# Optimization experiments

Measured on AMD Instinct MI355X. Metric: run time of the kernel, lower is better.

Reference implementation:

```python
import jax, jax.numpy as jnp
import numpy as np

B, S, D = 2, 2048, 768
H = 12
HD = D // H  # 64
SCALE = HD ** -0.5


def setup_inputs() -> dict:
    key = jax.random.key(0)
    k1, k2, k3, k4, k5 = jax.random.split(key, 5)
    x = jax.random.normal(k1, (B, S, D), dtype=jnp.float32)
    w_qkv = jax.random.normal(k2, (D, 3 * D), dtype=jnp.float32) * (D ** -0.5)
    b_qkv = jax.random.normal(k3, (3 * D,), dtype=jnp.float32) * 0.02
    w_proj = jax.random.normal(k4, (D, D), dtype=jnp.float32) * (D ** -0.5)
    b_proj = jax.random.normal(k5, (D,), dtype=jnp.float32) * 0.02
    return {"x": x, "w_qkv": w_qkv, "b_qkv": b_qkv, "w_proj": w_proj, "b_proj": b_proj}


def reference(x, w_qkv, b_qkv, w_proj, b_proj):
    b, s, d = x.shape
    # QKV projection: (B,S,3D) -> (3,B,H,S,HD)
    qkv = x @ w_qkv + b_qkv
    qkv = qkv.reshape(b, s, 3, H, HD).transpose(2, 0, 3, 1, 4)
    q, k, v = qkv[0], qkv[1], qkv[2]
    q = q * SCALE
    # full NxN attention scores, as in the original module
    attn = jnp.einsum("bhqd,bhkd->bhqk", q, k)
    attn = jax.nn.softmax(attn, axis=-1)
    out = jnp.einsum("bhqk,bhkd->bhqd", attn, v)  # (B,H,S,HD)
    out = out.transpose(0, 2, 1, 3).reshape(b, s, d)
    return out @ w_proj + b_proj
```

## Files before the change

### kernel.cpp

```cpp
#include <hip/hip_runtime.h>
#include <hip/hip_bf16.h>

#define B_ 2
#define S_ 2048
#define D_ 768
#define H_ 12
#define HD_ 64
#define EXP2C_ 0.1803368801111244f

typedef __attribute__((ext_vector_type(8))) short bf16x8;
typedef __attribute__((ext_vector_type(8))) unsigned short u16x8;
typedef __attribute__((ext_vector_type(4))) float f32x4;

static __device__ __forceinline__ unsigned short f2bf(float x) {
    union { float f; unsigned u; } v; v.f = x;
    unsigned r = (v.u + 0x7FFFu + ((v.u >> 16) & 1u)) >> 16;
    return (unsigned short)r;
}
static __device__ __forceinline__ float bf2f(unsigned short h) {
    union { unsigned u; float f; } v; v.u = ((unsigned)h) << 16;
    return v.f;
}
static __device__ __forceinline__ float fexp2(float x) { return __builtin_exp2f(x); }

static __device__ __forceinline__ unsigned pk_bf16(float a, float b) {
    __hip_bfloat162 pk = __float22bfloat162_rn(make_float2(a, b));
    union { __hip_bfloat162 h; unsigned u; } v; v.h = pk;
    return v.u;
}

static __device__ __forceinline__ f32x4 mfma32(bf16x8 a, bf16x8 b, f32x4 c) {
    return __builtin_amdgcn_mfma_f32_16x16x32_bf16(a, b, c, 0, 0, 0);
}

typedef __attribute__((address_space(3))) unsigned int lds_u32;
typedef __attribute__((address_space(1))) const unsigned int glb_u32;
static __device__ __forceinline__ void glds16(const unsigned short* g, unsigned short* l) {
    __builtin_amdgcn_global_load_lds((glb_u32*)g, (lds_u32*)l, 16, 0, 0);
}

#define PREP_CONV_ 1536
#define PREP_TQKV_ 1728
#define PREP_TPRJ_ 576
__global__ __launch_bounds__(256) void prep_kernel(
    const float* __restrict__ x,      unsigned short* __restrict__ x16,
    const float* __restrict__ w_qkv,  unsigned short* __restrict__ wqkvT,
    const float* __restrict__ w_proj, unsigned short* __restrict__ wprojT)
{
    __shared__ float tile[32][33];
    const int bid = blockIdx.x, t = threadIdx.x;
    if (bid < PREP_CONV_) {
        const int i = (bid * 256 + t) * 8;
        float4 a0 = *(const float4*)(x + i);
        float4 a1 = *(const float4*)(x + i + 4);
        u16x8 s;
        s[0] = f2bf(a0.x); s[1] = f2bf(a0.y); s[2] = f2bf(a0.z); s[3] = f2bf(a0.w);
        s[4] = f2bf(a1.x); s[5] = f2bf(a1.y); s[6] = f2bf(a1.z); s[7] = f2bf(a1.w);
        *(u16x8*)(x16 + i) = s;
        return;
    }
    const float* w; unsigned short* wT; int N, bb;
    if (bid < PREP_CONV_ + PREP_TQKV_) { w = w_qkv; wT = wqkvT; N = 3 * D_; bb = bid - PREP_CONV_; }
    else                               { w = w_proj; wT = wprojT; N = D_;   bb = bid - PREP_CONV_ - PREP_TQKV_; }
    const int K = D_;
    const int nt = N / 32;
    const int n0 = (bb % nt) * 32, k0 = (bb / nt) * 32;
    const int tx = t & 31, ty = t >> 5;
#pragma unroll
    for (int i = 0; i < 4; i++)
        tile[ty + i * 8][tx] = w[(size_t)(k0 + ty + i * 8) * N + n0 + tx];
    __syncthreads();
#pragma unroll
    for (int i = 0; i < 4; i++)
        wT[(size_t)(n0 + ty + i * 8) * K + k0 + tx] = f2bf(tile[tx][ty + i * 8]);
}

template <int BN, bool OUT_F32>
__global__ __launch_bounds__(256) void gemm_bt_kernel(
    const unsigned short* __restrict__ A,
    const unsigned short* __restrict__ Bt,
    const float* __restrict__ bias,
    void* __restrict__ Cp,
    int M, int N, int K)
{
    __shared__ __align__(16) unsigned short As[128][32];
    __shared__ __align__(16) unsigned short Bs[BN][32];
    constexpr int NJ = BN / 32;

    const int t = threadIdx.x;
    const int w = t >> 6, lane = t & 63, quad = lane >> 4, l16 = lane & 15;
    const int n0 = blockIdx.x * BN, m0 = blockIdx.y * 128;
    const int mw = (w & 1) * 64, nw = (w >> 1) * (BN / 2);

    const f32x4 z = {0.f, 0.f, 0.f, 0.f};
    f32x4 acc[4][NJ];
#pragma unroll
    for (int i = 0; i < 4; i++)
#pragma unroll
        for (int j = 0; j < NJ; j++) acc[i][j] = z;

    for (int kk = 0; kk < K; kk += 32) {
#pragma unroll
        for (int it = 0; it < 2; it++) {
            const int c = t + it * 256, row = c >> 2, c8 = (c & 3) << 3;
            glds16(A + (size_t)(m0 + row) * K + kk + c8, &As[0][0] + c * 8);
        }
#pragma unroll
        for (int it = 0; it < BN / 64; it++) {
            const int c = t + it * 256, row = c >> 2, c8 = (c & 3) << 3;
            glds16(Bt + (size_t)(n0 + row) * K + kk + c8, &Bs[0][0] + c * 8);
        }
        __syncthreads();

        bf16x8 a[4], b[NJ];
#pragma unroll
        for (int i = 0; i < 4; i++)
            a[i] = *(const bf16x8*)(&As[mw + i * 16 + l16][quad * 8]);
#pragma unroll
        for (int j = 0; j < NJ; j++)
            b[j] = *(const bf16x8*)(&Bs[nw + j * 16 + l16][quad * 8]);
#pragma unroll
        for (int i = 0; i < 4; i++)
#pragma unroll
            for (int j = 0; j < NJ; j++)
                acc[i][j] = mfma32(a[i], b[j], acc[i][j]);
        __syncthreads();
    }

#pragma unroll
    for (int j = 0; j < NJ; j++) {
        const int col = n0 + nw + j * 16 + l16;
        const float bv = bias[col];
#pragma unroll
        for (int i = 0; i < 4; i++) {
#pragma unroll
            for (int r = 0; r < 4; r++) {
                const int row = m0 + mw + i * 16 + quad * 4 + r;
                const float v = acc[i][j][r] + bv;
                if (OUT_F32) ((float*)Cp)[(size_t)row * N + col] = v;
                else         ((unsigned short*)Cp)[(size_t)row * N + col] = f2bf(v);
            }
        }
    }
}

__global__ __launch_bounds__(256) void repack_v_kernel(
    const unsigned short* __restrict__ qkv,
    unsigned short* __restrict__ vt)
{
    __shared__ unsigned short T[64][65];
    const int t = threadIdx.x;
    const int bh = blockIdx.x, st = blockIdx.y;
    const int b = bh / H_, h = bh % H_;
    const unsigned short* src =
        qkv + (size_t)(b * S_ + st * 64) * (3 * D_) + 2 * D_ + h * HD_;

#pragma unroll
    for (int it = 0; it < 2; it++) {
        const int c = t + it * 256, sr = c >> 3, g = c & 7;
        u16x8 v = *(const u16x8*)(src + (size_t)sr * (3 * D_) + g * 8);
#pragma unroll
        for (int j = 0; j < 8; j++) T[sr][g * 8 + j] = v[j];
    }
    __syncthreads();
#pragma unroll
    for (int it = 0; it < 2; it++) {
        const int c = t + it * 256, hd = c >> 3, g = c & 7;
        u16x8 v;
#pragma unroll
        for (int j = 0; j < 8; j++) v[j] = T[g * 8 + j][hd];
        *(u16x8*)(vt + (size_t)(bh * HD_ + hd) * S_ + st * 64 + g * 8) = v;
    }
}

__global__ __launch_bounds__(256) void attn_kernel(
    const unsigned short* __restrict__ qkv,
    const unsigned short* __restrict__ vt,
    unsigned short* __restrict__ o)
{
    __shared__ __align__(16) unsigned short Ks[2][64][64];
    __shared__ __align__(16) unsigned short Vs[2][64][64];
    __shared__ __align__(16) unsigned short p_lds[4][16][72];

    const int t = threadIdx.x;
    const int w = t >> 6, lane = t & 63, quad = lane >> 4, l16 = lane & 15;
    const int h8 = l16 & 7;
    const int bh = blockIdx.x, qt = blockIdx.y;
    const int b = bh / H_, h = bh % H_;
    const int ld = 3 * D_;

    const unsigned short* qbase =
        qkv + (size_t)(b * S_ + qt * 64 + 16 * w + l16) * ld + h * HD_;
    u16x8 qr0 = *(const u16x8*)(qbase + quad * 8);
    u16x8 qr1 = *(const u16x8*)(qbase + 32 + quad * 8);
    bf16x8 qf0, qf1;
#pragma unroll
    for (int j = 0; j < 8; j++) {
        qf0[j] = (short)f2bf(bf2f(qr0[j]) * EXP2C_);
        qf1[j] = (short)f2bf(bf2f(qr1[j]) * EXP2C_);
    }

    const unsigned short* kbase = qkv + (size_t)(b * S_) * ld + D_ + h * HD_;
    const unsigned short* vbase = vt + (size_t)bh * HD_ * S_;

    const f32x4 z = {0.f, 0.f, 0.f, 0.f};
    f32x4 o_acc[4] = {z, z, z, z};
    f32x4 l4[4] = {z, z, z, z};

#pragma unroll
    for (int it = 0; it < 2; it++) {
        const int c = t + it * 256, row = c >> 3, g = c & 7, sg = g ^ (row & 7);
        *(u16x8*)(&Ks[0][row][sg * 8]) = *(const u16x8*)(kbase + (size_t)row * ld + g * 8);
        *(u16x8*)(&Vs[0][row][sg * 8]) = *(const u16x8*)(vbase + (size_t)row * S_ + g * 8);
    }
    __syncthreads();

    const int NT = S_ / 64;
    for (int kt = 0; kt < NT; kt++) {
        const int buf = kt & 1;
        const bool pre = (kt + 1 < NT);

        u16x8 pk[2], pv[2];
        if (pre) {
            const int kr1 = (kt + 1) * 64;
#pragma unroll
            for (int i = 0; i < 2; i++) {
                const int c = t + i * 256, row = c >> 3, g = c & 7;
                pk[i] = *(const u16x8*)(kbase + (size_t)(kr1 + row) * ld + g * 8);
                pv[i] = *(const u16x8*)(vbase + (size_t)row * S_ + kr1 + g * 8);
            }
        }

        f32x4 s_acc[4] = {z, z, z, z};
#pragma unroll
        for (int nt = 0; nt < 4; nt++) {
            const unsigned short* kr = &Ks[buf][nt * 16 + l16][0];
            bf16x8 k0 = *(const bf16x8*)(kr + (quad ^ h8) * 8);
            bf16x8 k1 = *(const bf16x8*)(kr + ((quad + 4) ^ h8) * 8);
            s_acc[nt] = mfma32(qf0, k0, s_acc[nt]);
            s_acc[nt] = mfma32(qf1, k1, s_acc[nt]);
        }

#pragma unroll
        for (int nt = 0; nt < 4; nt++) {
            f32x4 pv4;
#pragma unroll
            for (int r = 0; r < 4; r++) pv4[r] = fexp2(s_acc[nt][r]);
            l4[nt] += pv4;
            const unsigned u01 = pk_bf16(pv4[0], pv4[1]);
            const unsigned u23 = pk_bf16(pv4[2], pv4[3]);
            p_lds[w][quad * 4 + 0][nt * 16 + l16] = (unsigned short)u01;
            p_lds[w][quad * 4 + 1][nt * 16 + l16] = (unsigned short)(u01 >> 16);
            p_lds[w][quad * 4 + 2][nt * 16 + l16] = (unsigned short)u23;
            p_lds[w][quad * 4 + 3][nt * 16 + l16] = (unsigned short)(u23 >> 16);
        }
        bf16x8 pa0 = *(const bf16x8*)(&p_lds[w][l16][quad * 8]);
        bf16x8 pa1 = *(const bf16x8*)(&p_lds[w][l16][32 + quad * 8]);

#pragma unroll
        for (int nt = 0; nt < 4; nt++) {
            const int row = nt * 16 + l16;
            bf16x8 v0 = *(const bf16x8*)(&Vs[buf][row][(quad ^ h8) * 8]);
            bf16x8 v1 = *(const bf16x8*)(&Vs[buf][row][((quad + 4) ^ h8) * 8]);
            o_acc[nt] = mfma32(pa0, v0, o_acc[nt]);
            o_acc[nt] = mfma32(pa1, v1, o_acc[nt]);
        }

        if (pre) {
#pragma unroll
            for (int i = 0; i < 2; i++) {
                const int c = t + i * 256, row = c >> 3, g = c & 7, sg = g ^ (row & 7);
                *(u16x8*)(&Ks[buf ^ 1][row][sg * 8]) = pk[i];
                *(u16x8*)(&Vs[buf ^ 1][row][sg * 8]) = pv[i];
            }
        }
        __syncthreads();
    }

#pragma unroll
    for (int r = 0; r < 4; r++) {
        float l = l4[0][r] + l4[1][r] + l4[2][r] + l4[3][r];
        l += __shfl_xor(l, 1, 64); l += __shfl_xor(l, 2, 64);
        l += __shfl_xor(l, 4, 64); l += __shfl_xor(l, 8, 64);
        const float inv = 1.f / l;
        const int row = b * S_ + qt * 64 + 16 * w + quad * 4 + r;
        unsigned short* ob = o + (size_t)row * D_ + h * HD_;
#pragma unroll
        for (int nt = 0; nt < 4; nt++)
            ob[nt * 16 + l16] = f2bf(o_acc[nt][r] * inv);
    }
}

extern "C" void kernel_launch(void* const* d_in, const int* in_sizes, int n_in,
                              void* d_out, int out_size, void* d_ws, size_t ws_size,
                              hipStream_t stream) {
    const float* x      = (const float*)d_in[0];
    const float* w_qkv  = (const float*)d_in[1];
    const float* b_qkv  = (const float*)d_in[2];
    const float* w_proj = (const float*)d_in[3];
    const float* b_proj = (const float*)d_in[4];
    float* out = (float*)d_out;

    unsigned short* qkv    = (unsigned short*)d_ws;
    unsigned short* vtb    = qkv    + (size_t)(B_ * S_) * (3 * D_);
    unsigned short* o_x16  = vtb    + (size_t)(B_ * H_) * HD_ * S_;
    unsigned short* wqkvT  = o_x16  + (size_t)(B_ * S_) * D_;
    unsigned short* wprojT = wqkvT  + (size_t)D_ * (3 * D_);

    dim3 blk(256);
    prep_kernel<<<dim3(PREP_CONV_ + PREP_TQKV_ + PREP_TPRJ_), blk, 0, stream>>>(
        x, o_x16, w_qkv, wqkvT, w_proj, wprojT);
    gemm_bt_kernel<128, false><<<dim3((3 * D_) / 128, (B_ * S_) / 128), blk, 0, stream>>>(
        o_x16, wqkvT, b_qkv, qkv, B_ * S_, 3 * D_, D_);
    repack_v_kernel<<<dim3(B_ * H_, S_ / 64), blk, 0, stream>>>(qkv, vtb);
    attn_kernel<<<dim3(B_ * H_, S_ / 64), blk, 0, stream>>>(qkv, vtb, o_x16);
    gemm_bt_kernel<64, true><<<dim3(D_ / 64, (B_ * S_) / 128), blk, 0, stream>>>(
        o_x16, wprojT, b_proj, out, B_ * S_, D_, D_);
}
```

Baseline: 185.7 us.

## Switch attention to 32x32x16 MFMA with a 2x2 query/key wave split

```diff
diff --git a/kernel.cpp b/kernel.cpp
--- a/kernel.cpp
+++ b/kernel.cpp
@@ -11,26 +11,28 @@
 typedef __attribute__((ext_vector_type(8))) short bf16x8;
 typedef __attribute__((ext_vector_type(8))) unsigned short u16x8;
 typedef __attribute__((ext_vector_type(4))) float f32x4;
+typedef __attribute__((ext_vector_type(16))) float f32x16;
 
 static __device__ __forceinline__ unsigned short f2bf(float x) {
     union { float f; unsigned u; } v; v.f = x;
     unsigned r = (v.u + 0x7FFFu + ((v.u >> 16) & 1u)) >> 16;
     return (unsigned short)r;
 }
+static __device__ __forceinline__ unsigned short f2bf_fast(float x) {
+    union { float f; unsigned u; } v; v.f = x;
+    return (unsigned short)((v.u + 0x8000u) >> 16);
+}
 static __device__ __forceinline__ float bf2f(unsigned short h) {
     union { unsigned u; float f; } v; v.u = ((unsigned)h) << 16;
     return v.f;
 }
 static __device__ __forceinline__ float fexp2(float x) { return __builtin_exp2f(x); }
 
-static __device__ __forceinline__ unsigned pk_bf16(float a, float b) {
-    __hip_bfloat162 pk = __float22bfloat162_rn(make_float2(a, b));
-    union { __hip_bfloat162 h; unsigned u; } v; v.h = pk;
-    return v.u;
-}
-
 static __device__ __forceinline__ f32x4 mfma32(bf16x8 a, bf16x8 b, f32x4 c) {
     return __builtin_amdgcn_mfma_f32_16x16x32_bf16(a, b, c, 0, 0, 0);
+}
+static __device__ __forceinline__ f32x16 mfma3216(bf16x8 a, bf16x8 b, f32x16 c) {
+    return __builtin_amdgcn_mfma_f32_32x32x16_bf16(a, b, c, 0, 0, 0);
 }
 
 typedef __attribute__((address_space(3))) unsigned int lds_u32;
@@ -180,32 +182,31 @@
 {
     __shared__ __align__(16) unsigned short Ks[2][64][64];
     __shared__ __align__(16) unsigned short Vs[2][64][64];
-    __shared__ __align__(16) unsigned short p_lds[4][16][72];
+    __shared__ __align__(16) unsigned short p_lds[4][32][40];
 
     const int t = threadIdx.x;
-    const int w = t >> 6, lane = t & 63, quad = lane >> 4, l16 = lane & 15;
-    const int h8 = l16 & 7;
+    const int w = t >> 6, lane = t & 63;
+    const int l32 = lane & 31, lh = lane >> 5;
+    const int qg = w & 1, kg = w >> 1;
     const int bh = blockIdx.x, qt = blockIdx.y;
     const int b = bh / H_, h = bh % H_;
     const int ld = 3 * D_;
 
-    const unsigned short* qbase =
-        qkv + (size_t)(b * S_ + qt * 64 + 16 * w + l16) * ld + h * HD_;
-    u16x8 qr0 = *(const u16x8*)(qbase + quad * 8);
-    u16x8 qr1 = *(const u16x8*)(qbase + 32 + quad * 8);
-    bf16x8 qf0, qf1;
-#pragma unroll
-    for (int j = 0; j < 8; j++) {
-        qf0[j] = (short)f2bf(bf2f(qr0[j]) * EXP2C_);
-        qf1[j] = (short)f2bf(bf2f(qr1[j]) * EXP2C_);
+    const unsigned short* qb =
+        qkv + (size_t)(b * S_ + qt * 64 + qg * 32 + l32) * ld + h * HD_;
+    bf16x8 qa[4];
+#pragma unroll
+    for (int c = 0; c < 4; c++) {
+        u16x8 r = *(const u16x8*)(qb + c * 16 + lh * 8);
+#pragma unroll
+        for (int j = 0; j < 8; j++) qa[c][j] = (short)f2bf(bf2f(r[j]) * EXP2C_);
     }
 
     const unsigned short* kbase = qkv + (size_t)(b * S_) * ld + D_ + h * HD_;
     const unsigned short* vbase = vt + (size_t)bh * HD_ * S_;
 
-    const f32x4 z = {0.f, 0.f, 0.f, 0.f};
-    f32x4 o_acc[4] = {z, z, z, z};
-    f32x4 l4[4] = {z, z, z, z};
+    f32x16 o0 = {0.f}, o1 = {0.f};
+    f32x4 l4[4] = {{0.f,0.f,0.f,0.f},{0.f,0.f,0.f,0.f},{0.f,0.f,0.f,0.f},{0.f,0.f,0.f,0.f}};
 
 #pragma unroll
     for (int it = 0; it < 2; it++) {
@@ -231,39 +232,41 @@
             }
         }
 
-        f32x4 s_acc[4] = {z, z, z, z};
-#pragma unroll
-        for (int nt = 0; nt < 4; nt++) {
-            const unsigned short* kr = &Ks[buf][nt * 16 + l16][0];
-            bf16x8 k0 = *(const bf16x8*)(kr + (quad ^ h8) * 8);
-            bf16x8 k1 = *(const bf16x8*)(kr + ((quad + 4) ^ h8) * 8);
-            s_acc[nt] = mfma32(qf0, k0, s_acc[nt]);
-            s_acc[nt] = mfma32(qf1, k1, s_acc[nt]);
-        }
-
-#pragma unroll
-        for (int nt = 0; nt < 4; nt++) {
-            f32x4 pv4;
-#pragma unroll
-            for (int r = 0; r < 4; r++) pv4[r] = fexp2(s_acc[nt][r]);
-            l4[nt] += pv4;
-            const unsigned u01 = pk_bf16(pv4[0], pv4[1]);
-            const unsigned u23 = pk_bf16(pv4[2], pv4[3]);
-            p_lds[w][quad * 4 + 0][nt * 16 + l16] = (unsigned short)u01;
-            p_lds[w][quad * 4 + 1][nt * 16 + l16] = (unsigned short)(u01 >> 16);
-            p_lds[w][quad * 4 + 2][nt * 16 + l16] = (unsigned short)u23;
-            p_lds[w][quad * 4 + 3][nt * 16 + l16] = (unsigned short)(u23 >> 16);
-        }
-        bf16x8 pa0 = *(const bf16x8*)(&p_lds[w][l16][quad * 8]);
-        bf16x8 pa1 = *(const bf16x8*)(&p_lds[w][l16][32 + quad * 8]);
-
-#pragma unroll
-        for (int nt = 0; nt < 4; nt++) {
-            const int row = nt * 16 + l16;
-            bf16x8 v0 = *(const bf16x8*)(&Vs[buf][row][(quad ^ h8) * 8]);
-            bf16x8 v1 = *(const bf16x8*)(&Vs[buf][row][((quad + 4) ^ h8) * 8]);
-            o_acc[nt] = mfma32(pa0, v0, o_acc[nt]);
-            o_acc[nt] = mfma32(pa1, v1, o_acc[nt]);
+        f32x16 s = {0.f};
+        {
+            const int krow = kg * 32 + l32;
+            const unsigned short* kr = &Ks[buf][krow][0];
+#pragma unroll
+            for (int c = 0; c < 4; c++) {
+                const int gh = c * 2 + lh;
+                bf16x8 kb = *(const bf16x8*)(kr + ((gh ^ (krow & 7)) * 8));
+                s = mfma3216(qa[c], kb, s);
+            }
+        }
+
+#pragma unroll
+        for (int r = 0; r < 16; r++) {
+            const float p = fexp2(s[r]);
+            l4[r >> 2][r & 3] += p;
+            const int qrow = (r & 3) + 8 * (r >> 2) + 4 * lh;
+            p_lds[w][qrow][l32] = f2bf_fast(p);
+        }
+        bf16x8 pf0 = *(const bf16x8*)(&p_lds[w][l32][lh * 8]);
+        bf16x8 pf1 = *(const bf16x8*)(&p_lds[w][l32][16 + lh * 8]);
+
+        {
+            const int r0 = l32, r1 = 32 + l32;
+            const unsigned short* v0 = &Vs[buf][r0][0];
+            const unsigned short* v1 = &Vs[buf][r1][0];
+            const int g0 = kg * 4 + lh, g1 = kg * 4 + 2 + lh;
+            bf16x8 va = *(const bf16x8*)(v0 + ((g0 ^ (r0 & 7)) * 8));
+            bf16x8 vb = *(const bf16x8*)(v0 + ((g1 ^ (r0 & 7)) * 8));
+            bf16x8 vc = *(const bf16x8*)(v1 + ((g0 ^ (r1 & 7)) * 8));
+            bf16x8 vd = *(const bf16x8*)(v1 + ((g1 ^ (r1 & 7)) * 8));
+            o0 = mfma3216(pf0, va, o0);
+            o0 = mfma3216(pf1, vb, o0);
+            o1 = mfma3216(pf0, vc, o1);
+            o1 = mfma3216(pf1, vd, o1);
         }
 
         if (pre) {
@@ -277,17 +280,46 @@
         __syncthreads();
     }
 
-#pragma unroll
-    for (int r = 0; r < 4; r++) {
-        float l = l4[0][r] + l4[1][r] + l4[2][r] + l4[3][r];
-        l += __shfl_xor(l, 1, 64); l += __shfl_xor(l, 2, 64);
-        l += __shfl_xor(l, 4, 64); l += __shfl_xor(l, 8, 64);
-        const float inv = 1.f / l;
-        const int row = b * S_ + qt * 64 + 16 * w + quad * 4 + r;
-        unsigned short* ob = o + (size_t)row * D_ + h * HD_;
-#pragma unroll
-        for (int nt = 0; nt < 4; nt++)
-            ob[nt * 16 + l16] = f2bf(o_acc[nt][r] * inv);
+    f32x4* K4 = (f32x4*)(&Ks[0][0][0]);
+    f32x4* P4 = (f32x4*)(&p_lds[0][0][0]);
+    const int sl = qg * 64 + lane;
+    if (kg == 1) {
+#pragma unroll
+        for (int c = 0; c < 4; c++) {
+            f32x4 t0 = {o0[c*4+0], o0[c*4+1], o0[c*4+2], o0[c*4+3]};
+            f32x4 t1 = {o1[c*4+0], o1[c*4+1], o1[c*4+2], o1[c*4+3]};
+            K4[c * 128 + sl] = t0;
+            K4[(c + 4) * 128 + sl] = t1;
+            P4[c * 128 + sl] = l4[c];
+        }
+    }
+    __syncthreads();
+    if (kg == 0) {
+#pragma unroll
+        for (int c = 0; c < 4; c++) {
+            f32x4 t0 = K4[c * 128 + sl];
+            f32x4 t1 = K4[(c + 4) * 128 + sl];
+            f32x4 tl = P4[c * 128 + sl];
+#pragma unroll
+            for (int j = 0; j < 4; j++) {
+                o0[c*4+j] += t0[j];
+                o1[c*4+j] += t1[j];
+            }
+            l4[c] += tl;
+        }
+#pragma unroll
+        for (int r = 0; r < 16; r++) {
+            float l = l4[r >> 2][r & 3];
+            l += __shfl_xor(l, 1, 64);  l += __shfl_xor(l, 2, 64);
+            l += __shfl_xor(l, 4, 64);  l += __shfl_xor(l, 8, 64);
+            l += __shfl_xor(l, 16, 64);
+            const float inv = 1.f / l;
+            const int qrow = (r & 3) + 8 * (r >> 2) + 4 * lh;
+            unsigned short* ob =
+                o + (size_t)(b * S_ + qt * 64 + qg * 32 + qrow) * D_ + h * HD_;
+            ob[l32]      = f2bf(o0[r] * inv);
+            ob[32 + l32] = f2bf(o1[r] * inv);
+        }
     }
 }
 
```

New measurement: 196.8 us. +6.0%, slower.
